# Optimization experiments

Hardware: AMD Instinct MI355X
Metric: run time of the kernel (lower is better)

## Reference

```python
import jax, jax.numpy as jnp
import numpy as np

N = 8192
D = 256
K = 32


def setup_inputs() -> dict:
    key = jax.random.key(0)
    kA, kX = jax.random.split(key)
    A = jax.random.normal(kA, (N, N), dtype=jnp.float32)
    X = jax.random.normal(kX, (N, D), dtype=jnp.float32)
    alpha = jnp.float32(0.3)  # nn.Parameter init value
    return {"A": A, "X": X, "alpha": alpha, "k": K}


def reference(A, X, alpha, k):
    # top-k mask along last dim: 1.0 at the k largest entries of each row
    _, topk_idx = jax.lax.top_k(A, k)  # [N, k]
    rows = jnp.arange(A.shape[0])[:, None]  # [N, 1]
    mask = jnp.zeros_like(A).at[rows, topk_idx].set(1.0)  # [N, N]
    # masked aggregation + residual: X + alpha * (mask @ X)
    X_agg = mask @ X  # [N, D]
    return X + alpha * X_agg
```

## Files before the change

kernel.cpp:

```cpp
#include <hip/hip_runtime.h>
#include <stdint.h>

#define NDIM 8192
#define DDIM 256
#define CAP  2048
#define MAXK 64

__device__ inline uint32_t f2key(float f) {
    uint32_t u = __float_as_uint(f);
    return (u & 0x80000000u) ? ~u : (u | 0x80000000u);
}

__global__ __launch_bounds__(256) void topk_agg_kernel(
    const float* __restrict__ A, const float* __restrict__ X,
    const float* __restrict__ alpha_p, const int* __restrict__ k_p,
    float* __restrict__ out)
{
    const int row  = blockIdx.x;
    const int tid  = threadIdx.x;
    const int lane = tid & 63;
    const int wid  = tid >> 6;

    __shared__ unsigned long long cand[CAP];
    __shared__ int s_count;
    __shared__ int s_sel[MAXK];
    __shared__ unsigned long long s_red[4];

    int k = *k_p;
    if (k > MAXK) k = MAXK;
    const float alpha = *alpha_p;

    const float* __restrict__ rowp = A + (size_t)row * NDIM;

    const float xres = X[(size_t)row * DDIM + tid];

    float4 v0, v1, v2, v3, v4, v5, v6, v7;
    {
        const float4* p = reinterpret_cast<const float4*>(rowp);
        v0 = p[0 * 256 + tid];
        v1 = p[1 * 256 + tid];
        v2 = p[2 * 256 + tid];
        v3 = p[3 * 256 + tid];
        v4 = p[4 * 256 + tid];
        v5 = p[5 * 256 + tid];
        v6 = p[6 * 256 + tid];
        v7 = p[7 * 256 + tid];
    }

    const float thrs[6] = {2.5f, 2.0f, 3.2f, 1.2f, 0.0f, -2.0f};
    bool ok = false;
    int count = 0;

    for (int ti = 0; ti < 6 && !ok; ++ti) {
        const float thr = thrs[ti];
        if (tid == 0) s_count = 0;
        __syncthreads();

        #pragma unroll
        for (int i = 0; i < 8; ++i) {
            const float4 v = (i == 0) ? v0 : (i == 1) ? v1 : (i == 2) ? v2 :
                             (i == 3) ? v3 : (i == 4) ? v4 : (i == 5) ? v5 :
                             (i == 6) ? v6 : v7;
            const int base = (i * 256 + tid) * 4;
            #pragma unroll
            for (int c = 0; c < 4; ++c) {
                const float f = (c == 0) ? v.x : (c == 1) ? v.y :
                                (c == 2) ? v.z : v.w;
                if (f > thr) {
                    const int pos = atomicAdd(&s_count, 1);
                    if (pos < CAP) {
                        const int idx = base + c;
                        cand[pos] = ((unsigned long long)f2key(f) << 32) |
                                    (uint32_t)(~(uint32_t)idx);
                    }
                }
            }
        }
        __syncthreads();
        count = s_count;
        ok = (count >= k && count <= CAP);
        __syncthreads();
    }

    if (ok) {
        #pragma unroll
        for (int m = 0; m < CAP / 256; ++m) {
            const int i = m * 256 + tid;
            if (i < count) {
                const unsigned long long mykey = cand[i];
                int rank = 0;
                for (int j = 0; j < count; ++j)
                    rank += (cand[j] > mykey) ? 1 : 0;
                if (rank < k)
                    s_sel[rank] = (int)(~(uint32_t)(mykey & 0xFFFFFFFFull));
            }
        }
        __syncthreads();
    } else {
        for (int t = 0; t < k; ++t) {
            unsigned long long best = 0ull;
            for (int it = 0; it < NDIM / 256; ++it) {
                const int idx = it * 256 + tid;
                const float f = rowp[idx];
                bool taken = false;
                for (int s = 0; s < t; ++s) taken |= (s_sel[s] == idx);
                if (!taken) {
                    const unsigned long long comp =
                        ((unsigned long long)f2key(f) << 32) |
                        (uint32_t)(~(uint32_t)idx);
                    if (comp > best) best = comp;
                }
            }
            #pragma unroll
            for (int o = 32; o > 0; o >>= 1) {
                const unsigned long long other = __shfl_down(best, o, 64);
                if (other > best) best = other;
            }
            if (lane == 0) s_red[wid] = best;
            __syncthreads();
            if (tid == 0) {
                unsigned long long b = s_red[0];
                for (int w = 1; w < 4; ++w)
                    if (s_red[w] > b) b = s_red[w];
                s_sel[t] = (int)(~(uint32_t)(b & 0xFFFFFFFFull));
            }
            __syncthreads();
        }
    }

    float acc = 0.0f;
    for (int t = 0; t < k; ++t) {
        acc += X[(size_t)s_sel[t] * DDIM + tid];
    }
    out[(size_t)row * DDIM + tid] = xres + alpha * acc;
}

extern "C" void kernel_launch(void* const* d_in, const int* in_sizes, int n_in,
                              void* d_out, int out_size, void* d_ws, size_t ws_size,
                              hipStream_t stream) {
    const float* A     = (const float*)d_in[0];
    const float* X     = (const float*)d_in[1];
    const float* alpha = (const float*)d_in[2];
    const int*   k     = (const int*)d_in[3];
    float* out = (float*)d_out;

    topk_agg_kernel<<<NDIM, 256, 0, stream>>>(A, X, alpha, k, out);
}
```

Before: 76.13 us.

## Use nontemporal loads/stores, unroll rank loop, specialize k=32 gather, tweak threshold

Loads of the A row and the output store now use nontemporal builtins, which keeps streaming data from evicting X from cache. The rank-counting loop is unrolled by 8, and the k==32 gather uses four independent accumulators so more X loads are in flight at once. The first candidate threshold drops from 2.5 to 2.45, which lowers the chance that a row falls back to a later pass. The threshold is tuned to the normal-distributed test inputs, but fallbacks keep the result correct.

```diff
diff --git a/kernel.cpp b/kernel.cpp
--- a/kernel.cpp
+++ b/kernel.cpp
@@ -5,6 +5,8 @@
 #define DDIM 256
 #define CAP  2048
 #define MAXK 64
+
+typedef float v4f __attribute__((ext_vector_type(4)));
 
 __device__ inline uint32_t f2key(float f) {
     uint32_t u = __float_as_uint(f);
@@ -34,20 +36,20 @@
 
     const float xres = X[(size_t)row * DDIM + tid];
 
-    float4 v0, v1, v2, v3, v4, v5, v6, v7;
+    v4f v0, v1, v2, v3, v4, v5, v6, v7;
     {
-        const float4* p = reinterpret_cast<const float4*>(rowp);
-        v0 = p[0 * 256 + tid];
-        v1 = p[1 * 256 + tid];
-        v2 = p[2 * 256 + tid];
-        v3 = p[3 * 256 + tid];
-        v4 = p[4 * 256 + tid];
-        v5 = p[5 * 256 + tid];
-        v6 = p[6 * 256 + tid];
-        v7 = p[7 * 256 + tid];
+        const v4f* p = reinterpret_cast<const v4f*>(rowp);
+        v0 = __builtin_nontemporal_load(p + 0 * 256 + tid);
+        v1 = __builtin_nontemporal_load(p + 1 * 256 + tid);
+        v2 = __builtin_nontemporal_load(p + 2 * 256 + tid);
+        v3 = __builtin_nontemporal_load(p + 3 * 256 + tid);
+        v4 = __builtin_nontemporal_load(p + 4 * 256 + tid);
+        v5 = __builtin_nontemporal_load(p + 5 * 256 + tid);
+        v6 = __builtin_nontemporal_load(p + 6 * 256 + tid);
+        v7 = __builtin_nontemporal_load(p + 7 * 256 + tid);
     }
 
-    const float thrs[6] = {2.5f, 2.0f, 3.2f, 1.2f, 0.0f, -2.0f};
+    const float thrs[6] = {2.45f, 2.0f, 3.2f, 1.2f, 0.0f, -2.0f};
     bool ok = false;
     int count = 0;
 
@@ -58,14 +60,13 @@
 
         #pragma unroll
         for (int i = 0; i < 8; ++i) {
-            const float4 v = (i == 0) ? v0 : (i == 1) ? v1 : (i == 2) ? v2 :
-                             (i == 3) ? v3 : (i == 4) ? v4 : (i == 5) ? v5 :
-                             (i == 6) ? v6 : v7;
+            const v4f v = (i == 0) ? v0 : (i == 1) ? v1 : (i == 2) ? v2 :
+                          (i == 3) ? v3 : (i == 4) ? v4 : (i == 5) ? v5 :
+                          (i == 6) ? v6 : v7;
             const int base = (i * 256 + tid) * 4;
             #pragma unroll
             for (int c = 0; c < 4; ++c) {
-                const float f = (c == 0) ? v.x : (c == 1) ? v.y :
-                                (c == 2) ? v.z : v.w;
+                const float f = v[c];
                 if (f > thr) {
                     const int pos = atomicAdd(&s_count, 1);
                     if (pos < CAP) {
@@ -89,7 +90,21 @@
             if (i < count) {
                 const unsigned long long mykey = cand[i];
                 int rank = 0;
-                for (int j = 0; j < count; ++j)
+                int j = 0;
+                for (; j + 8 <= count; j += 8) {
+                    const unsigned long long c0 = cand[j + 0];
+                    const unsigned long long c1 = cand[j + 1];
+                    const unsigned long long c2 = cand[j + 2];
+                    const unsigned long long c3 = cand[j + 3];
+                    const unsigned long long c4 = cand[j + 4];
+                    const unsigned long long c5 = cand[j + 5];
+                    const unsigned long long c6 = cand[j + 6];
+                    const unsigned long long c7 = cand[j + 7];
+                    rank += (c0 > mykey) + (c1 > mykey) + (c2 > mykey) +
+                            (c3 > mykey) + (c4 > mykey) + (c5 > mykey) +
+                            (c6 > mykey) + (c7 > mykey);
+                }
+                for (; j < count; ++j)
                     rank += (cand[j] > mykey) ? 1 : 0;
                 if (rank < k)
                     s_sel[rank] = (int)(~(uint32_t)(mykey & 0xFFFFFFFFull));
@@ -128,11 +143,25 @@
         }
     }
 
-    float acc = 0.0f;
-    for (int t = 0; t < k; ++t) {
-        acc += X[(size_t)s_sel[t] * DDIM + tid];
+    float acc;
+    if (k == 32) {
+        float a0 = 0.f, a1 = 0.f, a2 = 0.f, a3 = 0.f;
+        #pragma unroll
+        for (int t = 0; t < 32; t += 4) {
+            const float g0 = X[(size_t)s_sel[t + 0] * DDIM + tid];
+            const float g1 = X[(size_t)s_sel[t + 1] * DDIM + tid];
+            const float g2 = X[(size_t)s_sel[t + 2] * DDIM + tid];
+            const float g3 = X[(size_t)s_sel[t + 3] * DDIM + tid];
+            a0 += g0; a1 += g1; a2 += g2; a3 += g3;
+        }
+        acc = (a0 + a1) + (a2 + a3);
+    } else {
+        acc = 0.f;
+        for (int t = 0; t < k; ++t)
+            acc += X[(size_t)s_sel[t] * DDIM + tid];
     }
-    out[(size_t)row * DDIM + tid] = xres + alpha * acc;
+    __builtin_nontemporal_store(xres + alpha * acc,
+                                out + (size_t)row * DDIM + tid);
 }
 
 extern "C" void kernel_launch(void* const* d_in, const int* in_sizes, int n_in,
```

New measurement: 68.06 us. 10.6% less time.
